# Kernel tuning notes

Measured on AMD Instinct MI355X. Metric: run time of the kernel, lower is better.

Reference implementation:

```python
import jax, jax.numpy as jnp
import numpy as np

IMG = 2048
STRIDES = [8, 16, 32, 64, 128]
A = 9                       # num_cell_anchors
CLASS_NUM = 16              # num_classes - 1
TOPK = 1000                 # config.test_layer_topk
MAX_DELTA = float(np.log(1000.0 / 16.0))

_LEVEL_N = [(IMG // s) * (IMG // s) * A for s in STRIDES]


def setup_inputs() -> dict:
    key = jax.random.key(0)
    inp = {}
    for l, n in enumerate(_LEVEL_N):
        key, k1, k2, k3, k4 = jax.random.split(key, 5)
        cxcy = jax.random.uniform(k1, (n, 2), minval=0.0, maxval=float(IMG))
        wh = jax.random.uniform(k2, (n, 2), minval=8.0, maxval=128.0)
        inp[f"anchors{l}"] = jnp.concatenate([cxcy - 0.5 * wh, cxcy + 0.5 * wh], axis=1)
        # logits biased negative like a trained RetinaNet cls head (prior_prob init)
        inp[f"cls{l}"] = jax.random.normal(k3, (1, n, CLASS_NUM), dtype=jnp.float32) - 4.0
        inp[f"reg{l}"] = jax.random.normal(k4, (1, n, 8), dtype=jnp.float32) * 0.1
    return inp


def bbox_transform_inv(rois, deltas):
    # standard box decode (restore_bbox with unnormalize=False)
    w = rois[:, 2] - rois[:, 0]
    h = rois[:, 3] - rois[:, 1]
    cx = rois[:, 0] + 0.5 * w
    cy = rois[:, 1] + 0.5 * h
    pcx = cx + deltas[:, 0] * w
    pcy = cy + deltas[:, 1] * h
    pw = w * jnp.exp(jnp.minimum(deltas[:, 2], MAX_DELTA))
    ph = h * jnp.exp(jnp.minimum(deltas[:, 3], MAX_DELTA))
    return jnp.stack([pcx - 0.5 * pw, pcy - 0.5 * ph,
                      pcx + 0.5 * pw, pcy + 0.5 * ph], axis=1)


def _per_layer(anchors, pred_cls, pred_reg):
    a = anchors.reshape(-1, 4)
    c = pred_cls[0].reshape(-1, CLASS_NUM)
    r = pred_reg[0].reshape(-1, 8)[:, :4]
    if a.shape[0] > TOPK:
        ruler = jnp.max(c, axis=1)                  # max score over classes
        _, inds = jax.lax.top_k(ruler, TOPK)        # irregular topk + gather
        a = jnp.take(a, inds, axis=0)
        c = jnp.take(c, inds, axis=0)
        r = jnp.take(r, inds, axis=0)
    return a, jax.nn.sigmoid(c), r


def reference(anchors0, cls0, reg0, anchors1, cls1, reg1, anchors2, cls2, reg2,
              anchors3, cls3, reg3, anchors4, cls4, reg4):
    levels = [(anchors0, cls0, reg0), (anchors1, cls1, reg1),
              (anchors2, cls2, reg2), (anchors3, cls3, reg3),
              (anchors4, cls4, reg4)]
    kept = [_per_layer(a, c, r) for a, c, r in levels]
    keep_anchors = jnp.concatenate([k[0] for k in kept], axis=0)   # [K,4]
    keep_cls = jnp.concatenate([k[1] for k in kept], axis=0)       # [K,C]
    keep_reg = jnp.concatenate([k[2] for k in kept], axis=0)       # [K,4]
    K = keep_cls.shape[0]
    tag = jnp.tile(jnp.arange(CLASS_NUM, dtype=keep_cls.dtype) + 1.0, (K,)).reshape(-1, 1)
    pred_scores = keep_cls.reshape(-1, 1)                          # [K*C,1]
    pred_bbox = bbox_transform_inv(keep_anchors, keep_reg)         # [K,4]
    pred_bbox = jnp.tile(pred_bbox, (1, CLASS_NUM)).reshape(-1, 4) # [K*C,4]
    return jnp.concatenate([pred_bbox, pred_scores, tag], axis=1)  # [K*C,6]
```

## Files before the change

kernel.cpp:

```cpp
#include <hip/hip_runtime.h>
#include <math.h>

#define NLEV 5
#define TOPKK 1000
#define NCLS 16
#define NPART 16
#define HP 16u
#define PART_CAP 256
#define CAND_TOT 2048
#define NCHUNK 3069u
#define HISTSZ (NLEV * 256)
#define BAR_U32 5120u

__device__ __forceinline__ unsigned g_load(const unsigned* p) {
    return __hip_atomic_load(p, __ATOMIC_RELAXED, __HIP_MEMORY_SCOPE_AGENT);
}
__device__ __forceinline__ unsigned long long g_load64(const unsigned long long* p) {
    return __hip_atomic_load(p, __ATOMIC_RELAXED, __HIP_MEMORY_SCOPE_AGENT);
}
__device__ __forceinline__ void g_store(unsigned* p, unsigned v) {
    __hip_atomic_store(p, v, __ATOMIC_RELAXED, __HIP_MEMORY_SCOPE_AGENT);
}
__device__ __forceinline__ void g_store64(unsigned long long* p, unsigned long long v) {
    __hip_atomic_store(p, v, __ATOMIC_RELAXED, __HIP_MEMORY_SCOPE_AGENT);
}

__device__ __forceinline__ int lev_of_chunk(unsigned c) {
    if (c < 2304u) return 0;
    if (c < 2880u) return 1;
    if (c < 3024u) return 2;
    if (c < 3060u) return 3;
    return 4;
}
__device__ __forceinline__ unsigned lev_base(int l) {
    unsigned b = 0u;
    if (l == 1) b = 589824u;
    if (l == 2) b = 737280u;
    if (l == 3) b = 774144u;
    if (l == 4) b = 783360u;
    return b;
}

struct Ptrs {
    const float* anc[NLEV];
    const float* cls[NLEV];
    const float* reg[NLEV];
};

__device__ __forceinline__ unsigned f2key(float f) {
    unsigned u = __float_as_uint(f);
    return (u & 0x80000000u) ? ~u : (u | 0x80000000u);
}

__device__ __forceinline__ float max4(float4 v) {
    return fmaxf(fmaxf(v.x, v.y), fmaxf(v.z, v.w));
}

__device__ __forceinline__ void bar_arrive(unsigned* inst) {
    if (threadIdx.x == 0) g_store(inst + blockIdx.x, 1u);
}

template<unsigned NBV>
__device__ __forceinline__ void bar_monitor_fanout(unsigned* inst, unsigned* wsh) {
    const int t = threadIdx.x;
    for (;;) {
        unsigned f0 = g_load(inst + t);
        unsigned f1 = (256u + (unsigned)t < NBV) ? g_load(inst + 256 + t) : 1u;
        unsigned f2 = (NBV > 512u && 512u + (unsigned)t < NBV) ? g_load(inst + 512 + t) : 1u;
        unsigned f3 = (NBV > 768u && 768u + (unsigned)t < NBV) ? g_load(inst + 768 + t) : 1u;
        unsigned all = f0 & f1 & f2 & f3;
        unsigned long long bal = __ballot(all != 0u);
        if ((t & 63) == 0) wsh[t >> 6] = (bal == 0xFFFFFFFFFFFFFFFFull) ? 1u : 0u;
        __syncthreads();
        bool done = wsh[0] && wsh[1] && wsh[2] && wsh[3];
        __syncthreads();
        if (done) break;
        __builtin_amdgcn_s_sleep(1);
    }
    for (unsigned idx = (unsigned)t; idx < NBV; idx += 256u)
        g_store(inst + 1024u + idx * 4u, 1u);
}

__device__ __forceinline__ void bar_waitgo(unsigned* inst) {
    while (!g_load(inst + 1024u + blockIdx.x * 4u))
        __builtin_amdgcn_s_sleep(2);
}

template<unsigned NBV>
__device__ __forceinline__ void gridbar(unsigned* inst, unsigned* wsh) {
    __syncthreads();
    bar_arrive(inst);
    if (blockIdx.x == 0) {
        bar_monitor_fanout<NBV>(inst, wsh);
    } else if (threadIdx.x == 0) {
        bar_waitgo(inst);
    }
    __syncthreads();
}

__device__ __forceinline__ void sel256(unsigned c, unsigned rem,
                                       unsigned* wsum, unsigned* aux) {
    int t = threadIdx.x, lane = t & 63, wv = t >> 6;
    unsigned s = c;
    #pragma unroll
    for (int d = 1; d < 64; d <<= 1) {
        unsigned o = __shfl_down(s, d, 64);
        if (lane + d < 64) s += o;
    }
    if (lane == 0) wsum[wv] = s;
    __syncthreads();
    unsigned incl = s;
    #pragma unroll
    for (int w2 = 1; w2 < 4; w2++) if (wv + w2 < 4) incl += wsum[wv + w2];
    unsigned above = incl - c;
    if (above < rem && rem <= incl) {
        aux[0] = (unsigned)t;
        aux[1] = rem - above;
    }
    __syncthreads();
}

__device__ __forceinline__ unsigned hist_sum(const unsigned* hist, int lev) {
    unsigned vv[HP];
    #pragma unroll
    for (unsigned pp = 0; pp < HP; pp++)
        vv[pp] = g_load(hist + pp * HISTSZ + (unsigned)lev * 256u
                        + (unsigned)threadIdx.x);
    unsigned s = 0;
    #pragma unroll
    for (unsigned pp = 0; pp < HP; pp++) s += vv[pp];
    return s;
}

template<unsigned CPBV, unsigned NBV>
__global__ __launch_bounds__(256, 2) void k_fused(Ptrs p, unsigned* histA,
        unsigned* histB, unsigned* cnt, unsigned* bar,
        unsigned long long* cand, float* out) {
    __shared__ unsigned long long lbuf[CAND_TOT];
    __shared__ unsigned hh[256];
    __shared__ unsigned wsum[4];
    __shared__ unsigned wsh[4];
    __shared__ unsigned aux[33];

    const unsigned b = blockIdx.x;
    const int t = threadIdx.x;
    const unsigned c0 = b * CPBV;
    const int lev = lev_of_chunk(c0);
    const unsigned ebase = lev_base(lev);
    unsigned* bar0 = bar;
    unsigned* bar1 = bar + BAR_U32;
    unsigned* bar2 = bar + 2u * BAR_U32;

    unsigned keys[CPBV];
    const float4* f4p = (const float4*)(p.cls[lev]);
    #pragma unroll
    for (unsigned j = 0; j < CPBV; j++) {
        unsigned ch = c0 + j;
        unsigned k = 0u;
        if (ch < NCHUNK) {
            unsigned base4 = (ch * 256u - ebase) * 4u;
            float4 a0 = f4p[base4 + 0u * 256u + (unsigned)t];
            float4 a1 = f4p[base4 + 1u * 256u + (unsigned)t];
            float4 a2 = f4p[base4 + 2u * 256u + (unsigned)t];
            float4 a3 = f4p[base4 + 3u * 256u + (unsigned)t];
            float m0 = max4(a0), m1 = max4(a1), m2 = max4(a2), m3 = max4(a3);
            m0 = fmaxf(m0, __shfl_xor(m0, 1, 64));
            m0 = fmaxf(m0, __shfl_xor(m0, 2, 64));
            m1 = fmaxf(m1, __shfl_xor(m1, 1, 64));
            m1 = fmaxf(m1, __shfl_xor(m1, 2, 64));
            m2 = fmaxf(m2, __shfl_xor(m2, 1, 64));
            m2 = fmaxf(m2, __shfl_xor(m2, 2, 64));
            m3 = fmaxf(m3, __shfl_xor(m3, 1, 64));
            m3 = fmaxf(m3, __shfl_xor(m3, 2, 64));
            int g = t & 3;
            float mm = (g == 0) ? m0 : (g == 1) ? m1 : (g == 2) ? m2 : m3;
            k = f2key(mm);
        }
        keys[j] = k;
    }
    hh[t] = 0u;
    __syncthreads();
    #pragma unroll
    for (unsigned j = 0; j < CPBV; j++)
        if (c0 + j < NCHUNK) atomicAdd(&hh[keys[j] >> 24], 1u);
    __syncthreads();
    {
        unsigned v = hh[t];
        if (v) atomicAdd(&histA[(b & (HP - 1u)) * HISTSZ
                                + (unsigned)lev * 256u + (unsigned)t], v);
    }
    gridbar<NBV>(bar0, wsh);

    sel256(hist_sum(histA, lev), TOPKK, wsum, aux);
    unsigned binA = aux[0], remA = aux[1];
    __syncthreads();

    hh[t] = 0u;
    __syncthreads();
    #pragma unroll
    for (unsigned j = 0; j < CPBV; j++) {
        unsigned k = keys[j];
        if ((c0 + j) < NCHUNK && (k >> 24) == binA)
            atomicAdd(&hh[(k >> 16) & 0xFFu], 1u);
    }
    __syncthreads();
    {
        unsigned v = hh[t];
        if (v) atomicAdd(&histB[(b & (HP - 1u)) * HISTSZ
                                + (unsigned)lev * 256u + (unsigned)t], v);
    }
    gridbar<NBV>(bar1, wsh);

    sel256(hist_sum(histB, lev), remA, wsum, aux);
    unsigned thresh = (binA << 24) | (aux[0] << 16);
    __syncthreads();

    const unsigned eloc = (((unsigned)t & 3u) << 6) | ((unsigned)t >> 2);
    #pragma unroll
    for (unsigned j = 0; j < CPBV; j++) {
        unsigned ch = c0 + j;
        unsigned k = keys[j];
        if (ch < NCHUNK && k >= thresh) {
            unsigned loc = ch * 256u - ebase + eloc;
            unsigned part = ch & (NPART - 1u);
            unsigned slot = atomicAdd(&cnt[(lev * NPART + part) * 16u], 1u);
            if (slot < PART_CAP)
                g_store64(&cand[((size_t)(lev * NPART + part)) * PART_CAP + slot],
                          ((unsigned long long)k << 32) | (unsigned)(~loc));
        }
    }

    bool ranker = b < (unsigned)(NLEV * 8);
    __syncthreads();
    bar_arrive(bar2);
    if (b == 0) {
        bar_monitor_fanout<NBV>(bar2, wsh);
    } else if (ranker) {
        if (t == 0) bar_waitgo(bar2);
    } else {
        return;
    }
    __syncthreads();

    const float MAXD = 4.135166556742356f;
    int l = (int)(b >> 3);
    unsigned sl = b & 7u;

    if (t < NPART) {
        unsigned cc = g_load(cnt + (l * NPART + t) * 16u);
        aux[t] = (cc > PART_CAP) ? PART_CAP : cc;
    }
    __syncthreads();
    if (t == 0) {
        unsigned o = 0;
        for (int pp = 0; pp < NPART; pp++) { aux[16 + pp] = o; o += aux[pp]; }
        aux[32] = (o > CAND_TOT) ? CAND_TOT : o;
    }
    __syncthreads();
    unsigned n = aux[32];
    {
        unsigned long long tv[NPART];
        unsigned vok = 0u;
        #pragma unroll
        for (int pp = 0; pp < NPART; pp++) {
            bool ok = (unsigned)t < aux[pp];
            if (ok) tv[pp] = g_load64(&cand[((size_t)(l * NPART + pp)) * PART_CAP
                                            + (unsigned)t]);
            vok |= ok ? (1u << pp) : 0u;
        }
        #pragma unroll
        for (int pp = 0; pp < NPART; pp++) {
            if (vok & (1u << pp)) {
                unsigned dst = aux[16 + pp] + (unsigned)t;
                if (dst < CAND_TOT) lbuf[dst] = tv[pp];
            }
        }
    }
    __syncthreads();

    unsigned j = sl * 256u + (unsigned)t;
    if (j >= n) return;
    unsigned long long my = lbuf[j];
    unsigned rank = 0;
    #pragma unroll 8
    for (unsigned q = 0; q < n; q++) rank += (lbuf[q] > my) ? 1u : 0u;
    if (rank >= TOPKK) return;

    unsigned idx = ~((unsigned)(my & 0xFFFFFFFFull));
    float4 an = ((const float4*)p.anc[l])[idx];
    float4 dd = ((const float4*)p.reg[l])[(size_t)idx * 2];
    float w = an.z - an.x, h = an.w - an.y;
    float cx = an.x + 0.5f * w, cy = an.y + 0.5f * h;
    float pcx = cx + dd.x * w, pcy = cy + dd.y * h;
    float pw = w * expf(fminf(dd.z, MAXD));
    float ph = h * expf(fminf(dd.w, MAXD));
    float bx = pcx - 0.5f * pw, by = pcy - 0.5f * ph;
    float bz = pcx + 0.5f * pw, bw = pcy + 0.5f * ph;

    const float4* cp = (const float4*)(p.cls[l]) + (size_t)idx * 4;
    float sg[16];
    #pragma unroll
    for (int g = 0; g < 4; g++) {
        float4 v = cp[g];
        sg[4 * g + 0] = 1.0f / (1.0f + expf(-v.x));
        sg[4 * g + 1] = 1.0f / (1.0f + expf(-v.y));
        sg[4 * g + 2] = 1.0f / (1.0f + expf(-v.z));
        sg[4 * g + 3] = 1.0f / (1.0f + expf(-v.w));
    }
    float4* q = (float4*)(out + (size_t)(l * TOPKK + rank) * (NCLS * 6));
    #pragma unroll
    for (int g = 0; g < 8; g++) {
        float ta = (float)(2 * g + 1), tb = (float)(2 * g + 2);
        q[3 * g + 0] = make_float4(bx, by, bz, bw);
        q[3 * g + 1] = make_float4(sg[2 * g], ta, bx, by);
        q[3 * g + 2] = make_float4(bz, bw, sg[2 * g + 1], tb);
    }
}

extern "C" void kernel_launch(void* const* d_in, const int* in_sizes, int n_in,
                              void* d_out, int out_size, void* d_ws, size_t ws_size,
                              hipStream_t stream) {
    (void)in_sizes; (void)n_in; (void)out_size; (void)ws_size;
    Ptrs p;
    for (int l = 0; l < NLEV; l++) {
        p.anc[l] = (const float*)d_in[3 * l + 0];
        p.cls[l] = (const float*)d_in[3 * l + 1];
        p.reg[l] = (const float*)d_in[3 * l + 2];
    }

    static int s_which = -1;
    if (s_which < 0) {
        int bpcu = 0;
        if (hipOccupancyMaxActiveBlocksPerMultiprocessor(
                &bpcu, (const void*)k_fused<3u, 1023u>, 256, 0) != hipSuccess)
            bpcu = 0;
        int dev = 0, ncu = 0;
        (void)hipGetDevice(&dev);
        if (hipDeviceGetAttribute(&ncu, hipDeviceAttributeMultiprocessorCount,
                                  dev) != hipSuccess || ncu < 1)
            ncu = 0;
        s_which = (bpcu >= 4 && (long long)bpcu * ncu >= 1023) ? 1 : 0;
    }

    char* w = (char*)d_ws;
    unsigned* histA = (unsigned*)w;
    unsigned* histB = (unsigned*)(w + 81920);
    unsigned* cnt   = (unsigned*)(w + 163840);
    unsigned* bar   = (unsigned*)(w + 168960);
    unsigned long long* cand = (unsigned long long*)(w + 230400);
    float* out = (float*)d_out;

    (void)hipMemsetAsync(w, 0, 230400, stream);
    if (s_which == 1) {
        k_fused<3u, 1023u><<<dim3(1023), dim3(256), 0, stream>>>(
            p, histA, histB, cnt, bar, cand, out);
    } else {
        k_fused<6u, 512u><<<dim3(512), dim3(256), 0, stream>>>(
            p, histA, histB, cnt, bar, cand, out);
    }
}
```

Baseline: 163.4 us.

## Replace per-call workspace memset with epoch-tagged barriers and double-buffered self-cleaning state

Moves the histogram, counter, barrier and candidate scratch into static device globals. A global epoch counter tags the barrier flags, so they no longer need zeroing, and the histogram and counter buffers are double-buffered. The running kernel zeroes the other copy for the next call. This removes the separate hipMemsetAsync launch before each kernel and drops the chunk-range checks in the 1023-block variant. It relies on calls being serialized on one device and on the epoch being updated correctly, and the first call depends on the globals being zero-initialized.

```diff
diff --git a/kernel.cpp b/kernel.cpp
--- a/kernel.cpp
+++ b/kernel.cpp
@@ -10,7 +10,16 @@
 #define CAND_TOT 2048
 #define NCHUNK 3069u
 #define HISTSZ (NLEV * 256)
+#define HIST_U32 (HP * HISTSZ)
+#define CNT_U32 (NLEV * NPART * 16)
 #define BAR_U32 5120u
+#define CLEAN_U32 (2u * HIST_U32 + CNT_U32)
+
+__device__ unsigned g_epoch;
+__device__ unsigned g_bar[3u * BAR_U32];
+__device__ unsigned g_hist[2][2][HIST_U32];
+__device__ unsigned g_cnt[2][CNT_U32];
+__device__ unsigned long long g_cand[NLEV * NPART * PART_CAP];
 
 __device__ __forceinline__ unsigned g_load(const unsigned* p) {
     return __hip_atomic_load(p, __ATOMIC_RELAXED, __HIP_MEMORY_SCOPE_AGENT);
@@ -56,20 +65,21 @@
     return fmaxf(fmaxf(v.x, v.y), fmaxf(v.z, v.w));
 }
 
-__device__ __forceinline__ void bar_arrive(unsigned* inst) {
-    if (threadIdx.x == 0) g_store(inst + blockIdx.x, 1u);
+__device__ __forceinline__ void bar_arrive(unsigned* inst, unsigned tag) {
+    if (threadIdx.x == 0) g_store(inst + blockIdx.x, tag);
 }
 
 template<unsigned NBV>
-__device__ __forceinline__ void bar_monitor_fanout(unsigned* inst, unsigned* wsh) {
+__device__ __forceinline__ void bar_monitor_fanout(unsigned* inst, unsigned* wsh,
+                                                   unsigned tag) {
     const int t = threadIdx.x;
     for (;;) {
         unsigned f0 = g_load(inst + t);
-        unsigned f1 = (256u + (unsigned)t < NBV) ? g_load(inst + 256 + t) : 1u;
-        unsigned f2 = (NBV > 512u && 512u + (unsigned)t < NBV) ? g_load(inst + 512 + t) : 1u;
-        unsigned f3 = (NBV > 768u && 768u + (unsigned)t < NBV) ? g_load(inst + 768 + t) : 1u;
-        unsigned all = f0 & f1 & f2 & f3;
-        unsigned long long bal = __ballot(all != 0u);
+        unsigned f1 = (256u + (unsigned)t < NBV) ? g_load(inst + 256 + t) : tag;
+        unsigned f2 = (NBV > 512u && 512u + (unsigned)t < NBV) ? g_load(inst + 512 + t) : tag;
+        unsigned f3 = (NBV > 768u && 768u + (unsigned)t < NBV) ? g_load(inst + 768 + t) : tag;
+        bool all = (f0 == tag) && (f1 == tag) && (f2 == tag) && (f3 == tag);
+        unsigned long long bal = __ballot(all);
         if ((t & 63) == 0) wsh[t >> 6] = (bal == 0xFFFFFFFFFFFFFFFFull) ? 1u : 0u;
         __syncthreads();
         bool done = wsh[0] && wsh[1] && wsh[2] && wsh[3];
@@ -78,22 +88,22 @@
         __builtin_amdgcn_s_sleep(1);
     }
     for (unsigned idx = (unsigned)t; idx < NBV; idx += 256u)
-        g_store(inst + 1024u + idx * 4u, 1u);
-}
-
-__device__ __forceinline__ void bar_waitgo(unsigned* inst) {
-    while (!g_load(inst + 1024u + blockIdx.x * 4u))
+        g_store(inst + 1024u + idx * 4u, tag);
+}
+
+__device__ __forceinline__ void bar_waitgo(unsigned* inst, unsigned tag) {
+    while (g_load(inst + 1024u + blockIdx.x * 4u) != tag)
         __builtin_amdgcn_s_sleep(2);
 }
 
 template<unsigned NBV>
-__device__ __forceinline__ void gridbar(unsigned* inst, unsigned* wsh) {
-    __syncthreads();
-    bar_arrive(inst);
+__device__ __forceinline__ void gridbar(unsigned* inst, unsigned* wsh, unsigned tag) {
+    __syncthreads();
+    bar_arrive(inst, tag);
     if (blockIdx.x == 0) {
-        bar_monitor_fanout<NBV>(inst, wsh);
+        bar_monitor_fanout<NBV>(inst, wsh, tag);
     } else if (threadIdx.x == 0) {
-        bar_waitgo(inst);
+        bar_waitgo(inst, tag);
     }
     __syncthreads();
 }
@@ -133,9 +143,7 @@
 }
 
 template<unsigned CPBV, unsigned NBV>
-__global__ __launch_bounds__(256, 2) void k_fused(Ptrs p, unsigned* histA,
-        unsigned* histB, unsigned* cnt, unsigned* bar,
-        unsigned long long* cand, float* out) {
+__global__ __launch_bounds__(256, 2) void k_fused(Ptrs p, float* out) {
     __shared__ unsigned long long lbuf[CAND_TOT];
     __shared__ unsigned hh[256];
     __shared__ unsigned wsum[4];
@@ -147,9 +155,16 @@
     const unsigned c0 = b * CPBV;
     const int lev = lev_of_chunk(c0);
     const unsigned ebase = lev_base(lev);
-    unsigned* bar0 = bar;
-    unsigned* bar1 = bar + BAR_U32;
-    unsigned* bar2 = bar + 2u * BAR_U32;
+
+    const unsigned e   = g_load(&g_epoch);
+    const unsigned tag = e + 1u;
+    const unsigned bk  = e & 1u;
+    unsigned* histA = g_hist[bk][0];
+    unsigned* histB = g_hist[bk][1];
+    unsigned* cnt   = g_cnt[bk];
+    unsigned* bar0 = g_bar;
+    unsigned* bar1 = g_bar + BAR_U32;
+    unsigned* bar2 = g_bar + 2u * BAR_U32;
 
     unsigned keys[CPBV];
     const float4* f4p = (const float4*)(p.cls[lev]);
@@ -157,7 +172,8 @@
     for (unsigned j = 0; j < CPBV; j++) {
         unsigned ch = c0 + j;
         unsigned k = 0u;
-        if (ch < NCHUNK) {
+        bool inr = (CPBV == 3u) ? true : (ch < NCHUNK);
+        if (inr) {
             unsigned base4 = (ch * 256u - ebase) * 4u;
             float4 a0 = f4p[base4 + 0u * 256u + (unsigned)t];
             float4 a1 = f4p[base4 + 1u * 256u + (unsigned)t];
@@ -182,14 +198,14 @@
     __syncthreads();
     #pragma unroll
     for (unsigned j = 0; j < CPBV; j++)
-        if (c0 + j < NCHUNK) atomicAdd(&hh[keys[j] >> 24], 1u);
+        if (CPBV == 3u || c0 + j < NCHUNK) atomicAdd(&hh[keys[j] >> 24], 1u);
     __syncthreads();
     {
         unsigned v = hh[t];
         if (v) atomicAdd(&histA[(b & (HP - 1u)) * HISTSZ
                                 + (unsigned)lev * 256u + (unsigned)t], v);
     }
-    gridbar<NBV>(bar0, wsh);
+    gridbar<NBV>(bar0, wsh, tag);
 
     sel256(hist_sum(histA, lev), TOPKK, wsum, aux);
     unsigned binA = aux[0], remA = aux[1];
@@ -200,7 +216,7 @@
     #pragma unroll
     for (unsigned j = 0; j < CPBV; j++) {
         unsigned k = keys[j];
-        if ((c0 + j) < NCHUNK && (k >> 24) == binA)
+        if ((CPBV == 3u || (c0 + j) < NCHUNK) && (k >> 24) == binA)
             atomicAdd(&hh[(k >> 16) & 0xFFu], 1u);
     }
     __syncthreads();
@@ -209,7 +225,7 @@
         if (v) atomicAdd(&histB[(b & (HP - 1u)) * HISTSZ
                                 + (unsigned)lev * 256u + (unsigned)t], v);
     }
-    gridbar<NBV>(bar1, wsh);
+    gridbar<NBV>(bar1, wsh, tag);
 
     sel256(hist_sum(histB, lev), remA, wsum, aux);
     unsigned thresh = (binA << 24) | (aux[0] << 16);
@@ -220,23 +236,32 @@
     for (unsigned j = 0; j < CPBV; j++) {
         unsigned ch = c0 + j;
         unsigned k = keys[j];
-        if (ch < NCHUNK && k >= thresh) {
+        if ((CPBV == 3u || ch < NCHUNK) && k >= thresh) {
             unsigned loc = ch * 256u - ebase + eloc;
             unsigned part = ch & (NPART - 1u);
             unsigned slot = atomicAdd(&cnt[(lev * NPART + part) * 16u], 1u);
             if (slot < PART_CAP)
-                g_store64(&cand[((size_t)(lev * NPART + part)) * PART_CAP + slot],
+                g_store64(&g_cand[((size_t)(lev * NPART + part)) * PART_CAP + slot],
                           ((unsigned long long)k << 32) | (unsigned)(~loc));
         }
     }
 
+    {
+        unsigned bk1 = bk ^ 1u;
+        for (unsigned i = b * 256u + (unsigned)t; i < CLEAN_U32; i += NBV * 256u) {
+            if (i < 2u * HIST_U32) g_store(&g_hist[bk1][0][0] + i, 0u);
+            else                   g_store(&g_cnt[bk1][i - 2u * HIST_U32], 0u);
+        }
+    }
+
     bool ranker = b < (unsigned)(NLEV * 8);
     __syncthreads();
-    bar_arrive(bar2);
+    bar_arrive(bar2, tag);
     if (b == 0) {
-        bar_monitor_fanout<NBV>(bar2, wsh);
+        bar_monitor_fanout<NBV>(bar2, wsh, tag);
+        if (t == 0) g_store(&g_epoch, tag);
     } else if (ranker) {
-        if (t == 0) bar_waitgo(bar2);
+        if (t == 0) bar_waitgo(bar2, tag);
     } else {
         return;
     }
@@ -264,8 +289,8 @@
         #pragma unroll
         for (int pp = 0; pp < NPART; pp++) {
             bool ok = (unsigned)t < aux[pp];
-            if (ok) tv[pp] = g_load64(&cand[((size_t)(l * NPART + pp)) * PART_CAP
-                                            + (unsigned)t]);
+            if (ok) tv[pp] = g_load64(&g_cand[((size_t)(l * NPART + pp)) * PART_CAP
+                                              + (unsigned)t]);
             vok |= ok ? (1u << pp) : 0u;
         }
         #pragma unroll
@@ -320,7 +345,7 @@
 extern "C" void kernel_launch(void* const* d_in, const int* in_sizes, int n_in,
                               void* d_out, int out_size, void* d_ws, size_t ws_size,
                               hipStream_t stream) {
-    (void)in_sizes; (void)n_in; (void)out_size; (void)ws_size;
+    (void)in_sizes; (void)n_in; (void)out_size; (void)d_ws; (void)ws_size;
     Ptrs p;
     for (int l = 0; l < NLEV; l++) {
         p.anc[l] = (const float*)d_in[3 * l + 0];
@@ -342,20 +367,10 @@
         s_which = (bpcu >= 4 && (long long)bpcu * ncu >= 1023) ? 1 : 0;
     }
 
-    char* w = (char*)d_ws;
-    unsigned* histA = (unsigned*)w;
-    unsigned* histB = (unsigned*)(w + 81920);
-    unsigned* cnt   = (unsigned*)(w + 163840);
-    unsigned* bar   = (unsigned*)(w + 168960);
-    unsigned long long* cand = (unsigned long long*)(w + 230400);
     float* out = (float*)d_out;
-
-    (void)hipMemsetAsync(w, 0, 230400, stream);
     if (s_which == 1) {
-        k_fused<3u, 1023u><<<dim3(1023), dim3(256), 0, stream>>>(
-            p, histA, histB, cnt, bar, cand, out);
+        k_fused<3u, 1023u><<<dim3(1023), dim3(256), 0, stream>>>(p, out);
     } else {
-        k_fused<6u, 512u><<<dim3(512), dim3(256), 0, stream>>>(
-            p, histA, histB, cnt, bar, cand, out);
-    }
-}
+        k_fused<6u, 512u><<<dim3(512), dim3(256), 0, stream>>>(p, out);
+    }
+}
```

Result: no change. 164.7 us (+0.8%).
